# Performance work log

Measured on AMD Instinct MI355X. Metric: run time of the kernel, lower is better.

## Reference

```python
import jax, jax.numpy as jnp
import numpy as np

COMMITMENT_COST = 0.25


def setup_inputs() -> dict:
    key = jax.random.key(0)
    k1, k2 = jax.random.split(key)
    z_e = jax.random.normal(k1, (32, 64, 64, 64), dtype=jnp.float32)  # [B, C, H, W]
    emb = jax.random.normal(k2, (1024, 64), dtype=jnp.float32)        # [K, D] codebook
    return {"z_e": z_e, "emb": emb}


def reference(z_e, emb):
    B, C, H, W = z_e.shape
    K, D = emb.shape
    # [B, C, H, W] -> [B, H, W, C] -> [N, D]
    z = jnp.transpose(z_e, (0, 2, 3, 1))
    z_flat = z.reshape(-1, D)
    # squared L2 distances: ||z||^2 + ||e||^2 - 2 z e^T  -> [N, K]
    distances = (jnp.sum(z_flat * z_flat, axis=1, keepdims=True)
                 + jnp.sum(emb * emb, axis=1)
                 - 2.0 * (z_flat @ emb.T))
    indices = jnp.argmin(distances, axis=1)               # [N]
    encodings = jax.nn.one_hot(indices, K, dtype=z_flat.dtype)  # [N, K]
    quantized = emb[indices].reshape(z.shape)             # [B, H, W, D]
    # commitment loss (codebook is frozen / EMA-updated, so quantized is detached)
    loss = COMMITMENT_COST * jnp.mean((jax.lax.stop_gradient(quantized) - z) ** 2)
    # straight-through estimator
    quantized_st = z + jax.lax.stop_gradient(quantized - z)
    avg_probs = jnp.mean(encodings, axis=0)               # [K]
    perplexity = jnp.exp(-jnp.sum(avg_probs * jnp.log(avg_probs + 1e-10)))
    out = jnp.transpose(quantized_st, (0, 3, 1, 2))       # back to [B, C, H, W]
    return out, loss, perplexity, encodings
```

## Files before the change

### kernel.cpp

```cpp
#include <hip/hip_runtime.h>

typedef __attribute__((ext_vector_type(8)))  __bf16 bf16x8;
typedef __attribute__((ext_vector_type(16))) float  f32x16;

#define NPTS   131072
#define KCODES 1024
#define DDIM   64
#define HWSZ   4096

#define LOSS_OFF    8388608
#define PERP_OFF    8388609
#define ENC_OFF     8388610


__device__ __forceinline__ unsigned rnhi(float x) {
    unsigned u = __float_as_uint(x);
    return (u + 0x7fffu + ((u >> 16) & 1u)) & 0xffff0000u;
}

__device__ __forceinline__ void split3(float x, unsigned short& h1, unsigned short& h2, unsigned short& h3) {
    unsigned a = rnhi(x); float r1 = x - __uint_as_float(a);
    unsigned b = rnhi(r1); float r2 = r1 - __uint_as_float(b);
    unsigned c = rnhi(r2);
    h1 = (unsigned short)(a >> 16);
    h2 = (unsigned short)(b >> 16);
    h3 = (unsigned short)(c >> 16);
}

__global__ __launch_bounds__(256) void e2_kernel(const float* __restrict__ emb,
                                                 float* __restrict__ e2,
                                                 int* __restrict__ hist) {
    int k = blockIdx.x * 256 + threadIdx.x;
    hist[k] = 0;
    const float4* r = (const float4*)(emb + (size_t)k * DDIM);
    float s0 = 0.f, s1 = 0.f, s2 = 0.f, s3 = 0.f;
#pragma unroll
    for (int i = 0; i < 16; ++i) {
        float4 v = r[i];
        s0 = fmaf(v.x, v.x, s0);
        s1 = fmaf(v.y, v.y, s1);
        s2 = fmaf(v.z, v.z, s2);
        s3 = fmaf(v.w, v.w, s3);
    }
    e2[k] = (s0 + s1) + (s2 + s3);
}

__global__ __launch_bounds__(512, 4) void vq_mfma(
    const float* __restrict__ z_e, const float* __restrict__ emb,
    const float* __restrict__ e2g, float* __restrict__ out,
    float* __restrict__ enc, int* __restrict__ hist,
    float* __restrict__ blockLoss)
{
    __shared__ unsigned short planeA[3 * 8 * 1024];
    __shared__ float se2[KCODES];
    __shared__ int   sidx[256];
    __shared__ float swsum[8];

    const int tid  = threadIdx.x, bid = blockIdx.x;
    const int lane = tid & 63,    wid = tid >> 6;
    const int hi   = lane >> 5,   col = lane & 31;

    for (int i = tid; i < KCODES; i += 512) se2[i] = e2g[i];

    float* encSlice = enc + (size_t)bid * 256 * KCODES;
    float4* encF4   = (float4*)(encSlice + 2);

    const int n  = bid * 256 + wid * 32 + col;
    const int b  = n >> 12, hw = n & (HWSZ - 1);
    const float* zp = z_e + (size_t)b * (DDIM * HWSZ) + hw;

    bf16x8 Bv[3][4];
    float zzp = 0.f;
#pragma unroll
    for (int kk = 0; kk < 4; ++kk) {
        union { unsigned u[4]; bf16x8 v; } p1, p2, p3;
#pragma unroll
        for (int m = 0; m < 4; ++m) {
            float x0 = zp[(size_t)(16 * kk + 8 * hi + 2 * m    ) * HWSZ];
            float x1 = zp[(size_t)(16 * kk + 8 * hi + 2 * m + 1) * HWSZ];
            zzp = fmaf(x0, x0, zzp);
            zzp = fmaf(x1, x1, zzp);
            unsigned short a0, b0, c0, a1, b1, c1;
            split3(x0, a0, b0, c0);
            split3(x1, a1, b1, c1);
            p1.u[m] = (unsigned)a0 | ((unsigned)a1 << 16);
            p2.u[m] = (unsigned)b0 | ((unsigned)b1 << 16);
            p3.u[m] = (unsigned)c0 | ((unsigned)c1 << 16);
        }
        Bv[0][kk] = p1.v; Bv[1][kk] = p2.v; Bv[2][kk] = p3.v;
    }

    float best = 3.4e38f;
    int   bestk = 0;

    for (int chunk = 0; chunk < 8; ++chunk) {
        __syncthreads();
#pragma unroll
        for (int it = 0; it < 2; ++it) {
            const int code = tid & 127;
            const int sl   = (tid >> 7) + 4 * it;
            const float4* ep = (const float4*)(emb + (size_t)(chunk * 128 + code) * DDIM + sl * 8);
            float4 va = ep[0], vb = ep[1];
            float xs[8] = {va.x, va.y, va.z, va.w, vb.x, vb.y, vb.z, vb.w};
            unsigned w1[4], w2[4], w3[4];
#pragma unroll
            for (int m = 0; m < 4; ++m) {
                unsigned short a0, b0, c0, a1, b1, c1;
                split3(-2.f * xs[2 * m    ], a0, b0, c0);
                split3(-2.f * xs[2 * m + 1], a1, b1, c1);
                w1[m] = (unsigned)a0 | ((unsigned)a1 << 16);
                w2[m] = (unsigned)b0 | ((unsigned)b1 << 16);
                w3[m] = (unsigned)c0 | ((unsigned)c1 << 16);
            }
            const int off = sl * 1024 + code * 8;
            *(uint4*)&planeA[0 * 8192 + off] = make_uint4(w1[0], w1[1], w1[2], w1[3]);
            *(uint4*)&planeA[1 * 8192 + off] = make_uint4(w2[0], w2[1], w2[2], w2[3]);
            *(uint4*)&planeA[2 * 8192 + off] = make_uint4(w3[0], w3[1], w3[2], w3[3]);
        }
        __syncthreads();

        {
            const float4 z4 = make_float4(0.f, 0.f, 0.f, 0.f);
            const int base = chunk * 8192 + tid;
#pragma unroll
            for (int it = 0; it < 16; ++it) {
                const int idx = base + it * 512;
                if (idx < 65535) encF4[idx] = z4;
            }
            if (chunk == 0) {
                if (tid == 0) *(float2*)encSlice = make_float2(0.f, 0.f);
                if (tid == 1) *(float2*)(encSlice + 262142) = make_float2(0.f, 0.f);
            }
        }

        for (int t = 0; t < 4; ++t) {
            f32x16 acc0 = {0.f,0.f,0.f,0.f,0.f,0.f,0.f,0.f,0.f,0.f,0.f,0.f,0.f,0.f,0.f,0.f};
            f32x16 acc1 = {0.f,0.f,0.f,0.f,0.f,0.f,0.f,0.f,0.f,0.f,0.f,0.f,0.f,0.f,0.f,0.f};
            const int arow = (32 * t + col) * 8;
#pragma unroll
            for (int kk = 0; kk < 4; ++kk) {
                const int sb = (2 * kk + hi) * 1024 + arow;
                bf16x8 a1 = *(const bf16x8*)&planeA[0 * 8192 + sb];
                bf16x8 a2 = *(const bf16x8*)&planeA[1 * 8192 + sb];
                bf16x8 a3 = *(const bf16x8*)&planeA[2 * 8192 + sb];
                acc0 = __builtin_amdgcn_mfma_f32_32x32x16_bf16(a1, Bv[0][kk], acc0, 0, 0, 0);
                acc1 = __builtin_amdgcn_mfma_f32_32x32x16_bf16(a1, Bv[1][kk], acc1, 0, 0, 0);
                acc0 = __builtin_amdgcn_mfma_f32_32x32x16_bf16(a2, Bv[0][kk], acc0, 0, 0, 0);
                acc1 = __builtin_amdgcn_mfma_f32_32x32x16_bf16(a2, Bv[1][kk], acc1, 0, 0, 0);
                acc0 = __builtin_amdgcn_mfma_f32_32x32x16_bf16(a1, Bv[2][kk], acc0, 0, 0, 0);
                acc1 = __builtin_amdgcn_mfma_f32_32x32x16_bf16(a3, Bv[0][kk], acc1, 0, 0, 0);
                acc0 = __builtin_amdgcn_mfma_f32_32x32x16_bf16(a2, Bv[2][kk], acc0, 0, 0, 0);
                acc1 = __builtin_amdgcn_mfma_f32_32x32x16_bf16(a3, Bv[1][kk], acc1, 0, 0, 0);
            }
            const int cbase = chunk * 128 + 32 * t + 4 * hi;
#pragma unroll
            for (int r = 0; r < 16; ++r) {
                const int row  = (r & 3) + 8 * (r >> 2);
                const int code = cbase + row;
                const float sc = (acc0[r] + acc1[r]) + se2[code];
                if (sc < best) { best = sc; bestk = code; }
            }
        }
    }

    float obest = __shfl_down(best, 32);
    int   oidx  = __shfl_down(bestk, 32);
    float ozz   = __shfl_down(zzp, 32);
    if (obest < best || (obest == best && oidx < bestk)) { best = obest; bestk = oidx; }
    const float zz = zzp + ozz;
    float contrib = (lane < 32) ? (best + zz) : 0.f;
    if (lane < 32) {
        sidx[wid * 32 + col] = bestk;
        atomicAdd(&hist[bestk], 1);
    }
#pragma unroll
    for (int off = 32; off > 0; off >>= 1) contrib += __shfl_down(contrib, off);
    if (lane == 0) swsum[wid] = contrib;
    __syncthreads();
    if (tid == 0) {
        float s = 0.f;
        for (int i = 0; i < 8; ++i) s += swsum[i];
        blockLoss[bid] = s;
    }

    if (lane < 32) {
        const int nn = bid * 256 + wid * 32 + col;
        enc[(size_t)nn * KCODES + bestk] = 1.0f;
    }

    {
        const int i  = tid & 255, c0 = (tid >> 8) * 32;
        const int k  = sidx[i];
        const int nn = bid * 256 + i, bb = nn >> 12, hh = nn & (HWSZ - 1);
        const float4* er = (const float4*)(emb + (size_t)k * DDIM + c0);
        float* ob = out + (size_t)bb * (DDIM * HWSZ) + hh;
#pragma unroll
        for (int m = 0; m < 8; ++m) {
            float4 q = er[m];
            ob[(size_t)(c0 + 4 * m    ) * HWSZ] = q.x;
            ob[(size_t)(c0 + 4 * m + 1) * HWSZ] = q.y;
            ob[(size_t)(c0 + 4 * m + 2) * HWSZ] = q.z;
            ob[(size_t)(c0 + 4 * m + 3) * HWSZ] = q.w;
        }
    }
}

__global__ __launch_bounds__(1024) void fin_kernel(const int* __restrict__ hist,
                                                   const float* __restrict__ blockLoss,
                                                   float* __restrict__ dout)
{
    __shared__ float redE[16];
    __shared__ float redL[16];
    const int t = threadIdx.x;

    float p = (float)hist[t] * (1.f / 131072.f);
    float term = p * logf(p + 1e-10f);
    float lv = (t < 512) ? blockLoss[t] : 0.f;
#pragma unroll
    for (int off = 32; off > 0; off >>= 1) {
        term += __shfl_down(term, off);
        lv   += __shfl_down(lv, off);
    }
    const int lane = t & 63, wid = t >> 6;
    if (lane == 0) { redE[wid] = term; redL[wid] = lv; }
    __syncthreads();
    if (t == 0) {
        float te = 0.f, tl = 0.f;
        for (int i = 0; i < 16; ++i) { te += redE[i]; tl += redL[i]; }
        dout[LOSS_OFF] = 0.25f * tl * (1.f / (131072.f * 64.f));
        dout[PERP_OFF] = expf(-te);
    }
}

extern "C" void kernel_launch(void* const* d_in, const int* in_sizes, int n_in,
                              void* d_out, int out_size, void* d_ws, size_t ws_size,
                              hipStream_t stream) {
    const float* z_e = (const float*)d_in[0];
    const float* emb = (const float*)d_in[1];
    float* out = (float*)d_out;
    float* enc = out + ENC_OFF;

    float* e2        = (float*)d_ws;
    int*   hist      = (int*)((char*)d_ws + 4096);
    float* blockLoss = (float*)((char*)d_ws + 8192);

    e2_kernel<<<4, 256, 0, stream>>>(emb, e2, hist);
    vq_mfma<<<NPTS / 256, 512, 0, stream>>>(z_e, emb, e2, out, enc, hist, blockLoss);
    fin_kernel<<<1, 1024, 0, stream>>>(hist, blockLoss, out);
}
```

Baseline: 203.1 us.

## Split one-hot encoding writes into a separate streaming kernel

The zero-fill of the 512 MB one-hot encodings matrix, which was interleaved with the MFMA distance loop, moves out of the compute kernel. The compute kernel now stashes each row's argmin index in that row's first element of the encodings buffer. A new enc_write kernel reads those indices back and writes every full row with vectorized stores. Launch bounds drop from 4 to 2 blocks per CU. This separates the compute-bound and bandwidth-bound phases, but no longer lets the stores overlap with compute and adds a kernel launch.

```diff
diff --git a/kernel.cpp b/kernel.cpp
--- a/kernel.cpp
+++ b/kernel.cpp
@@ -45,7 +45,7 @@
     e2[k] = (s0 + s1) + (s2 + s3);
 }
 
-__global__ __launch_bounds__(512, 4) void vq_mfma(
+__global__ __launch_bounds__(512, 2) void vq_compute(
     const float* __restrict__ z_e, const float* __restrict__ emb,
     const float* __restrict__ e2g, float* __restrict__ out,
     float* __restrict__ enc, int* __restrict__ hist,
@@ -61,9 +61,6 @@
     const int hi   = lane >> 5,   col = lane & 31;
 
     for (int i = tid; i < KCODES; i += 512) se2[i] = e2g[i];
-
-    float* encSlice = enc + (size_t)bid * 256 * KCODES;
-    float4* encF4   = (float4*)(encSlice + 2);
 
     const int n  = bid * 256 + wid * 32 + col;
     const int b  = n >> 12, hw = n & (HWSZ - 1);
@@ -118,20 +115,6 @@
             *(uint4*)&planeA[2 * 8192 + off] = make_uint4(w3[0], w3[1], w3[2], w3[3]);
         }
         __syncthreads();
-
-        {
-            const float4 z4 = make_float4(0.f, 0.f, 0.f, 0.f);
-            const int base = chunk * 8192 + tid;
-#pragma unroll
-            for (int it = 0; it < 16; ++it) {
-                const int idx = base + it * 512;
-                if (idx < 65535) encF4[idx] = z4;
-            }
-            if (chunk == 0) {
-                if (tid == 0) *(float2*)encSlice = make_float2(0.f, 0.f);
-                if (tid == 1) *(float2*)(encSlice + 262142) = make_float2(0.f, 0.f);
-            }
-        }
 
         for (int t = 0; t < 4; ++t) {
             f32x16 acc0 = {0.f,0.f,0.f,0.f,0.f,0.f,0.f,0.f,0.f,0.f,0.f,0.f,0.f,0.f,0.f,0.f};
@@ -172,6 +155,7 @@
     if (lane < 32) {
         sidx[wid * 32 + col] = bestk;
         atomicAdd(&hist[bestk], 1);
+        ((int*)enc)[(size_t)n * KCODES] = bestk;
     }
 #pragma unroll
     for (int off = 32; off > 0; off >>= 1) contrib += __shfl_down(contrib, off);
@@ -183,11 +167,6 @@
         blockLoss[bid] = s;
     }
 
-    if (lane < 32) {
-        const int nn = bid * 256 + wid * 32 + col;
-        enc[(size_t)nn * KCODES + bestk] = 1.0f;
-    }
-
     {
         const int i  = tid & 255, c0 = (tid >> 8) * 32;
         const int k  = sidx[i];
@@ -201,6 +180,38 @@
             ob[(size_t)(c0 + 4 * m + 1) * HWSZ] = q.y;
             ob[(size_t)(c0 + 4 * m + 2) * HWSZ] = q.z;
             ob[(size_t)(c0 + 4 * m + 3) * HWSZ] = q.w;
+        }
+    }
+}
+
+__global__ __launch_bounds__(256) void enc_write(float* __restrict__ enc) {
+    __shared__ int rk[64];
+    const int t = threadIdx.x;
+    const int row0 = blockIdx.x * 64;
+
+    if (t < 64) rk[t] = ((const int*)enc)[(size_t)(row0 + t) * KCODES];
+    __syncthreads();
+
+    for (int r = 0; r < 64; ++r) {
+        const int k = rk[r];
+        float* rowp = enc + (size_t)(row0 + r) * KCODES;
+        if (t < 255) {
+            const int j = 2 + 4 * t;
+            float4 v;
+            v.x = (k == j    ) ? 1.f : 0.f;
+            v.y = (k == j + 1) ? 1.f : 0.f;
+            v.z = (k == j + 2) ? 1.f : 0.f;
+            v.w = (k == j + 3) ? 1.f : 0.f;
+            *(float4*)(rowp + j) = v;
+        } else {
+            float2 h;
+            h.x = (k == 0) ? 1.f : 0.f;
+            h.y = (k == 1) ? 1.f : 0.f;
+            *(float2*)rowp = h;
+            float2 tl;
+            tl.x = (k == 1022) ? 1.f : 0.f;
+            tl.y = (k == 1023) ? 1.f : 0.f;
+            *(float2*)(rowp + 1022) = tl;
         }
     }
 }
@@ -245,6 +256,7 @@
     float* blockLoss = (float*)((char*)d_ws + 8192);
 
     e2_kernel<<<4, 256, 0, stream>>>(emb, e2, hist);
-    vq_mfma<<<NPTS / 256, 512, 0, stream>>>(z_e, emb, e2, out, enc, hist, blockLoss);
+    vq_compute<<<NPTS / 256, 512, 0, stream>>>(z_e, emb, e2, out, enc, hist, blockLoss);
+    enc_write<<<NPTS / 64, 256, 0, stream>>>(enc);
     fin_kernel<<<1, 1024, 0, stream>>>(hist, blockLoss, out);
 }
```

Result: slower. 296.8 us (+46.2%).
